# Kernel optimization log

Measured on AMD Instinct MI355X. Metric: run time of the kernel, lower is better.

## Reference

```python
import jax, jax.numpy as jnp
import numpy as np

M_FEATS = 1536      # number of proposals (docstring: [M, K])
K_DIM = 128         # feature dim per docstring example
NUM_CLASSES = 16    # label vocabulary; torch.unique loop becomes a fixed class sweep


def setup_inputs() -> dict:
    key = jax.random.key(0)
    k1, k2 = jax.random.split(key)
    features = jax.random.normal(k1, (M_FEATS, K_DIM), dtype=jnp.float32)
    labels = jax.random.randint(k2, (M_FEATS,), 0, NUM_CLASSES, dtype=jnp.int32)
    # ious all ones -> keep = (ious >= 0.5) is all-True, so the boolean filter is identity
    ious = jnp.ones((M_FEATS,), dtype=jnp.float32)
    return {"features": features, "labels": labels, "ious": ious}


def reference(features, labels, ious):
    # reweight_func='none' -> coef = ones_like(ious); keep mask is all-True by construction
    coef = jnp.ones_like(ious)
    # similarity [M, M]; coef broadcasts over columns, matching `similarity * coef` in torch
    sim = jnp.matmul(features, features.T) * coef[None, :]
    m = sim.shape[0]
    eye = jnp.eye(m, dtype=sim.dtype)
    # ground set term: logdet(similarity + 0.5 I)  (mask_ground is all ones)
    ground = jnp.linalg.slogdet(sim + 0.5 * eye)[1]

    # Per-label logdet of the submatrix S_c + 0.5 I_{n_c}. Instead of extracting a
    # variable-size submatrix (not jit-able), embed it in a full [M, M] matrix that is
    # block-diagonal: class block = S_c + 0.5 I, off-class diagonal = 1. Its logdet
    # equals logdet(S_c + 0.5 I). Absent classes give identity -> logdet 0, matching
    # torch.unique skipping them.
    onehot = (labels[:, None] == jnp.arange(NUM_CLASSES, dtype=labels.dtype)[None, :])
    onehot = onehot.astype(sim.dtype)  # [M, C]

    def class_logdet(mask):  # mask: [M] 0/1 indicator for one class
        A = sim * (mask[:, None] * mask[None, :]) + jnp.diag(0.5 * mask + (1.0 - mask))
        return jnp.linalg.slogdet(A)[1]

    per_class = jax.vmap(class_logdet)(onehot.T)  # [C]
    loss = jnp.sum(per_class) - ground
    return loss  # scalar; .mean() of a scalar is itself
```

## Files before the change

kernel.cpp:

```cpp
#include <hip/hip_runtime.h>
#include <math.h>


#define M_FEATS 1536
#define K_DIM 128
#define NUM_CLASSES 16
#define SLICE 96
#define GRAM_ELEMS (K_DIM * K_DIM)
#define PIDX(i) ((i) + ((i) >> 4))
#define SENT 0x13579BDF

__device__ __forceinline__ float chol128(
    float A[8][8], const int t, const int rg, const int cg,
    const int i0, const int j0,
    float4* panLo, float4* panHi, float4* wshLo, float4* wshHi)
{
    float logsum = 0.0f;

    if (rg == 0) {
#pragma unroll
        for (int q = 0; q < 8; ++q) {
            panLo[PIDX(j0 + q)] = make_float4(A[0][q], A[1][q], A[2][q], A[3][q]);
            panHi[PIDX(j0 + q)] = make_float4(A[4][q], A[5][q], A[6][q], A[7][q]);
        }
    }

#pragma unroll 1
    for (int s = 0; s < 16; ++s) {
        const int k = 8 * s;
        __syncthreads();

        if (t < K_DIM) {
            float4 dL[8], dH[8];
#pragma unroll
            for (int c = 0; c < 8; ++c) {
                dL[c] = panLo[PIDX(k + c)];
                dH[c] = panHi[PIDX(k + c)];
            }
            float4 aL = panLo[PIDX(t)], aH = panHi[PIDX(t)];

            float D[8][8];
#pragma unroll
            for (int c = 0; c < 8; ++c) {
                D[0][c] = dL[c].x; D[1][c] = dL[c].y;
                D[2][c] = dL[c].z; D[3][c] = dL[c].w;
                D[4][c] = dH[c].x; D[5][c] = dH[c].y;
                D[6][c] = dH[c].z; D[7][c] = dH[c].w;
            }

            float L[8][8], ic[8];
            float prod = 1.0f;
#pragma unroll
            for (int c = 0; c < 8; ++c) {
                float v = D[c][c];
#pragma unroll
                for (int m = 0; m < c; ++m) v = fmaf(-L[c][m], L[c][m], v);
                prod *= v;
                ic[c] = rsqrtf(v);
#pragma unroll
                for (int r = c + 1; r < 8; ++r) {
                    float x = D[r][c];
#pragma unroll
                    for (int m = 0; m < c; ++m) x = fmaf(-L[r][m], L[c][m], x);
                    L[r][c] = x * ic[c];
                }
            }
            if (t == 0) logsum += logf(prod);

            float a[8] = {aL.x, aL.y, aL.z, aL.w, aH.x, aH.y, aH.z, aH.w};
            float w[8];
#pragma unroll
            for (int c = 0; c < 8; ++c) {
                float x = a[c];
#pragma unroll
                for (int m = 0; m < c; ++m) x = fmaf(-L[c][m], w[m], x);
                w[c] = x * ic[c];
            }
            wshLo[PIDX(t)] = make_float4(w[0], w[1], w[2], w[3]);
            wshHi[PIDX(t)] = make_float4(w[4], w[5], w[6], w[7]);
        }
        __syncthreads();

        if (rg > s && cg > s) {
            float4 wrL[8], wrH[8];
#pragma unroll
            for (int r = 0; r < 8; ++r) {
                wrL[r] = wshLo[PIDX(i0 + r)];
                wrH[r] = wshHi[PIDX(i0 + r)];
            }
#pragma unroll
            for (int q = 0; q < 8; ++q) {
                float4 wjL = wshLo[PIDX(j0 + q)];
                float4 wjH = wshHi[PIDX(j0 + q)];
#pragma unroll
                for (int r = 0; r < 8; ++r) {
                    float x = A[r][q];
                    x = fmaf(-wrL[r].x, wjL.x, x);
                    x = fmaf(-wrL[r].y, wjL.y, x);
                    x = fmaf(-wrL[r].z, wjL.z, x);
                    x = fmaf(-wrL[r].w, wjL.w, x);
                    x = fmaf(-wrH[r].x, wjH.x, x);
                    x = fmaf(-wrH[r].y, wjH.y, x);
                    x = fmaf(-wrH[r].z, wjH.z, x);
                    x = fmaf(-wrH[r].w, wjH.w, x);
                    A[r][q] = x;
                }
            }
        }
        if (rg == s + 1) {
#pragma unroll
            for (int q = 0; q < 8; ++q) {
                panLo[PIDX(j0 + q)] = make_float4(A[0][q], A[1][q], A[2][q], A[3][q]);
                panHi[PIDX(j0 + q)] = make_float4(A[4][q], A[5][q], A[6][q], A[7][q]);
            }
        }
    }
    return logsum;
}

__global__ __launch_bounds__(256, 1) void fused_kernel(
    const float* __restrict__ f, const int* __restrict__ labels,
    float* __restrict__ partials, float* __restrict__ groundG,
    int* __restrict__ flag1, int* __restrict__ flag2,
    float* __restrict__ ldet, int* __restrict__ flag3,
    float* __restrict__ out)
{
    __shared__ int cnt;
    __shared__ int list[M_FEATS];
    __shared__ float4 panLo[136], panHi[136], wshLo[136], wshHi[136];

    const int b = blockIdx.x;
    const int t = threadIdx.x;
    const int rg = t >> 4;
    const int cg = t & 15;
    const int i0 = rg << 3;
    const int j0 = cg << 3;

    float A[8][8];

    if (b < NUM_CLASSES) {
#pragma unroll
        for (int r = 0; r < 8; ++r)
#pragma unroll
            for (int q = 0; q < 8; ++q) A[r][q] = 0.0f;

        const float* base = f + (size_t)(SLICE * b) * K_DIM;
        float4 A0[3], A1[3], B0[3], B1[3];
#pragma unroll
        for (int u = 0; u < 3; ++u) {
            const float* rp = base + (size_t)u * K_DIM;
            A0[u] = *(const float4*)(rp + i0);
            A1[u] = *(const float4*)(rp + i0 + 4);
            B0[u] = *(const float4*)(rp + j0);
            B1[u] = *(const float4*)(rp + j0 + 4);
        }
        for (int jb = 0; jb < SLICE; jb += 3) {
#pragma unroll
            for (int u = 0; u < 3; ++u) {
                float fa[8] = {A0[u].x, A0[u].y, A0[u].z, A0[u].w,
                               A1[u].x, A1[u].y, A1[u].z, A1[u].w};
                float fb[8] = {B0[u].x, B0[u].y, B0[u].z, B0[u].w,
                               B1[u].x, B1[u].y, B1[u].z, B1[u].w};
#pragma unroll
                for (int r = 0; r < 8; ++r)
#pragma unroll
                    for (int q = 0; q < 8; ++q)
                        A[r][q] = fmaf(fa[r], fb[q], A[r][q]);
                int p = jb + u + 3;
                const float* rp = base + (size_t)(p < SLICE ? p : SLICE - 1) * K_DIM;
                A0[u] = *(const float4*)(rp + i0);
                A1[u] = *(const float4*)(rp + i0 + 4);
                B0[u] = *(const float4*)(rp + j0);
                B1[u] = *(const float4*)(rp + j0 + 4);
            }
        }

        float* g = partials + (size_t)b * GRAM_ELEMS;
#pragma unroll
        for (int r = 0; r < 8; ++r) {
            *(float4*)(g + (i0 + r) * K_DIM + j0) =
                make_float4(A[r][0], A[r][1], A[r][2], A[r][3]);
            *(float4*)(g + (i0 + r) * K_DIM + j0 + 4) =
                make_float4(A[r][4], A[r][5], A[r][6], A[r][7]);
        }
        __syncthreads();
        if (t == 0)
            __hip_atomic_store(&flag1[b], SENT, __ATOMIC_RELEASE,
                               __HIP_MEMORY_SCOPE_AGENT);

        if (t < NUM_CLASSES)
            while (__hip_atomic_load(&flag1[t], __ATOMIC_ACQUIRE,
                                     __HIP_MEMORY_SCOPE_AGENT) != SENT)
                __builtin_amdgcn_s_sleep(2);
        __syncthreads();

        {
            const int row = 8 * b + (t >> 5);
            const int col = (t & 31) << 2;
            float4 s = make_float4(0.f, 0.f, 0.f, 0.f);
#pragma unroll
            for (int c = 0; c < NUM_CLASSES; ++c) {
                float4 v = *(const float4*)(partials + (size_t)c * GRAM_ELEMS
                                            + row * K_DIM + col);
                s.x += v.x; s.y += v.y; s.z += v.z; s.w += v.w;
            }
            *(float4*)(groundG + row * K_DIM + col) = s;
        }
        __syncthreads();
        if (t == 0)
            __hip_atomic_store(&flag2[b], SENT, __ATOMIC_RELEASE,
                               __HIP_MEMORY_SCOPE_AGENT);
        return;
    }

    if (b < 2 * NUM_CLASSES) {
        const int cls = b - NUM_CLASSES;
        if (t == 0) cnt = 0;
        __syncthreads();
        for (int i = t; i < M_FEATS; i += 256)
            if (labels[i] == cls) list[atomicAdd(&cnt, 1)] = i;
        __syncthreads();
        const int n = cnt;

#pragma unroll
        for (int r = 0; r < 8; ++r)
#pragma unroll
            for (int q = 0; q < 8; ++q) A[r][q] = 0.0f;

        if (n > 0) {
            float4 A0[3], A1[3], B0[3], B1[3];
            int lidx[3];
#pragma unroll
            for (int u = 0; u < 3; ++u) {
                const float* rp = f + (size_t)list[u < n ? u : n - 1] * K_DIM;
                A0[u] = *(const float4*)(rp + i0);
                A1[u] = *(const float4*)(rp + i0 + 4);
                B0[u] = *(const float4*)(rp + j0);
                B1[u] = *(const float4*)(rp + j0 + 4);
                const int p = u + 3;
                lidx[u] = list[p < n ? p : n - 1];
            }
            for (int jb = 0; jb < n; jb += 3) {
#pragma unroll
                for (int u = 0; u < 3; ++u) {
                    if (jb + u < n) {
                        float fa[8] = {A0[u].x, A0[u].y, A0[u].z, A0[u].w,
                                       A1[u].x, A1[u].y, A1[u].z, A1[u].w};
                        float fb[8] = {B0[u].x, B0[u].y, B0[u].z, B0[u].w,
                                       B1[u].x, B1[u].y, B1[u].z, B1[u].w};
#pragma unroll
                        for (int r = 0; r < 8; ++r)
#pragma unroll
                            for (int q = 0; q < 8; ++q)
                                A[r][q] = fmaf(fa[r], fb[q], A[r][q]);
                    }
                    const float* rp = f + (size_t)lidx[u] * K_DIM;
                    A0[u] = *(const float4*)(rp + i0);
                    A1[u] = *(const float4*)(rp + i0 + 4);
                    B0[u] = *(const float4*)(rp + j0);
                    B1[u] = *(const float4*)(rp + j0 + 4);
                    const int p = jb + u + 6;
                    lidx[u] = list[p < n ? p : n - 1];
                }
            }
        }

#pragma unroll
        for (int r = 0; r < 8; ++r)
#pragma unroll
            for (int q = 0; q < 8; ++q)
                if ((i0 + r) == (j0 + q)) A[r][q] += 0.5f;

        float ls = chol128(A, t, rg, cg, i0, j0, panLo, panHi, wshLo, wshHi);

        if (t == 0) {
            ldet[cls] = ls;
            __hip_atomic_store(&flag3[cls], SENT, __ATOMIC_RELEASE,
                               __HIP_MEMORY_SCOPE_AGENT);
        }
        return;
    }

    if (t < NUM_CLASSES)
        while (__hip_atomic_load(&flag2[t], __ATOMIC_ACQUIRE,
                                 __HIP_MEMORY_SCOPE_AGENT) != SENT)
            __builtin_amdgcn_s_sleep(2);
    __syncthreads();

#pragma unroll
    for (int r = 0; r < 8; ++r) {
        float4 v0 = *(const float4*)(groundG + (i0 + r) * K_DIM + j0);
        float4 v1 = *(const float4*)(groundG + (i0 + r) * K_DIM + j0 + 4);
        A[r][0] = v0.x; A[r][1] = v0.y; A[r][2] = v0.z; A[r][3] = v0.w;
        A[r][4] = v1.x; A[r][5] = v1.y; A[r][6] = v1.z; A[r][7] = v1.w;
    }
#pragma unroll
    for (int r = 0; r < 8; ++r)
#pragma unroll
        for (int q = 0; q < 8; ++q)
            if ((i0 + r) == (j0 + q)) A[r][q] += 0.5f;

    float ls = chol128(A, t, rg, cg, i0, j0, panLo, panHi, wshLo, wshHi);

    if (t == 0) {
        float total = 1920.0f * 0.6931471805599453f - ls;
        for (int c = 0; c < NUM_CLASSES; ++c) {
            while (__hip_atomic_load(&flag3[c], __ATOMIC_ACQUIRE,
                                     __HIP_MEMORY_SCOPE_AGENT) != SENT)
                __builtin_amdgcn_s_sleep(2);
            total += ldet[c];
        }
        out[0] = total;
    }
}

extern "C" void kernel_launch(void* const* d_in, const int* in_sizes, int n_in,
                              void* d_out, int out_size, void* d_ws, size_t ws_size,
                              hipStream_t stream)
{
    const float* features = (const float*)d_in[0];
    const int* labels = (const int*)d_in[1];

    float* partials = (float*)d_ws;
    float* groundG  = partials + (size_t)NUM_CLASSES * GRAM_ELEMS;
    int* flag1      = (int*)(groundG + GRAM_ELEMS);
    int* flag2      = flag1 + NUM_CLASSES;
    float* ldetp    = (float*)(flag2 + NUM_CLASSES);
    int* flag3      = (int*)(ldetp + NUM_CLASSES);

    fused_kernel<<<2 * NUM_CLASSES + 1, 256, 0, stream>>>(
        features, labels, partials, groundG, flag1, flag2, ldetp, flag3,
        (float*)d_out);
}
```

Baseline: 108.0 us.

## Double threads per block to 512 with 4x8 per-thread tiles in Gram and Cholesky

Each block now runs 512 threads, and each thread holds a 4x8 register tile instead of 8x8. This halves per-thread work in the Gram accumulation and in the Cholesky trailing updates, and the panel write logic is split across pairs of row groups. The final block now polls the per-class flags in parallel instead of serially from one thread. The cost is more synchronization participants per barrier, and the panel-factor stage still uses only 128 threads.

```diff
diff --git a/kernel.cpp b/kernel.cpp
--- a/kernel.cpp
+++ b/kernel.cpp
@@ -11,7 +11,7 @@
 #define SENT 0x13579BDF
 
 __device__ __forceinline__ float chol128(
-    float A[8][8], const int t, const int rg, const int cg,
+    float A[4][8], const int t, const int rg, const int cg,
     const int i0, const int j0,
     float4* panLo, float4* panHi, float4* wshLo, float4* wshHi)
 {
@@ -19,10 +19,12 @@
 
     if (rg == 0) {
 #pragma unroll
-        for (int q = 0; q < 8; ++q) {
+        for (int q = 0; q < 8; ++q)
             panLo[PIDX(j0 + q)] = make_float4(A[0][q], A[1][q], A[2][q], A[3][q]);
-            panHi[PIDX(j0 + q)] = make_float4(A[4][q], A[5][q], A[6][q], A[7][q]);
-        }
+    } else if (rg == 1) {
+#pragma unroll
+        for (int q = 0; q < 8; ++q)
+            panHi[PIDX(j0 + q)] = make_float4(A[0][q], A[1][q], A[2][q], A[3][q]);
     }
 
 #pragma unroll 1
@@ -81,10 +83,10 @@
         }
         __syncthreads();
 
-        if (rg > s && cg > s) {
-            float4 wrL[8], wrH[8];
-#pragma unroll
-            for (int r = 0; r < 8; ++r) {
+        if (rg >= 2 * s + 2 && cg >= s + 1) {
+            float4 wrL[4], wrH[4];
+#pragma unroll
+            for (int r = 0; r < 4; ++r) {
                 wrL[r] = wshLo[PIDX(i0 + r)];
                 wrH[r] = wshHi[PIDX(i0 + r)];
             }
@@ -93,7 +95,7 @@
                 float4 wjL = wshLo[PIDX(j0 + q)];
                 float4 wjH = wshHi[PIDX(j0 + q)];
 #pragma unroll
-                for (int r = 0; r < 8; ++r) {
+                for (int r = 0; r < 4; ++r) {
                     float x = A[r][q];
                     x = fmaf(-wrL[r].x, wjL.x, x);
                     x = fmaf(-wrL[r].y, wjL.y, x);
@@ -107,18 +109,20 @@
                 }
             }
         }
-        if (rg == s + 1) {
-#pragma unroll
-            for (int q = 0; q < 8; ++q) {
+        if (rg == 2 * s + 2) {
+#pragma unroll
+            for (int q = 0; q < 8; ++q)
                 panLo[PIDX(j0 + q)] = make_float4(A[0][q], A[1][q], A[2][q], A[3][q]);
-                panHi[PIDX(j0 + q)] = make_float4(A[4][q], A[5][q], A[6][q], A[7][q]);
-            }
+        } else if (rg == 2 * s + 3) {
+#pragma unroll
+            for (int q = 0; q < 8; ++q)
+                panHi[PIDX(j0 + q)] = make_float4(A[0][q], A[1][q], A[2][q], A[3][q]);
         }
     }
     return logsum;
 }
 
-__global__ __launch_bounds__(256, 1) void fused_kernel(
+__global__ __launch_bounds__(512, 1) void fused_kernel(
     const float* __restrict__ f, const int* __restrict__ labels,
     float* __restrict__ partials, float* __restrict__ groundG,
     int* __restrict__ flag1, int* __restrict__ flag2,
@@ -133,43 +137,40 @@
     const int t = threadIdx.x;
     const int rg = t >> 4;
     const int cg = t & 15;
-    const int i0 = rg << 3;
+    const int i0 = rg << 2;
     const int j0 = cg << 3;
 
-    float A[8][8];
+    float A[4][8];
 
     if (b < NUM_CLASSES) {
 #pragma unroll
-        for (int r = 0; r < 8; ++r)
+        for (int r = 0; r < 4; ++r)
 #pragma unroll
             for (int q = 0; q < 8; ++q) A[r][q] = 0.0f;
 
         const float* base = f + (size_t)(SLICE * b) * K_DIM;
-        float4 A0[3], A1[3], B0[3], B1[3];
+        float4 Ar[3], B0[3], B1[3];
 #pragma unroll
         for (int u = 0; u < 3; ++u) {
             const float* rp = base + (size_t)u * K_DIM;
-            A0[u] = *(const float4*)(rp + i0);
-            A1[u] = *(const float4*)(rp + i0 + 4);
+            Ar[u] = *(const float4*)(rp + i0);
             B0[u] = *(const float4*)(rp + j0);
             B1[u] = *(const float4*)(rp + j0 + 4);
         }
         for (int jb = 0; jb < SLICE; jb += 3) {
 #pragma unroll
             for (int u = 0; u < 3; ++u) {
-                float fa[8] = {A0[u].x, A0[u].y, A0[u].z, A0[u].w,
-                               A1[u].x, A1[u].y, A1[u].z, A1[u].w};
+                float fa[4] = {Ar[u].x, Ar[u].y, Ar[u].z, Ar[u].w};
                 float fb[8] = {B0[u].x, B0[u].y, B0[u].z, B0[u].w,
                                B1[u].x, B1[u].y, B1[u].z, B1[u].w};
 #pragma unroll
-                for (int r = 0; r < 8; ++r)
+                for (int r = 0; r < 4; ++r)
 #pragma unroll
                     for (int q = 0; q < 8; ++q)
                         A[r][q] = fmaf(fa[r], fb[q], A[r][q]);
                 int p = jb + u + 3;
                 const float* rp = base + (size_t)(p < SLICE ? p : SLICE - 1) * K_DIM;
-                A0[u] = *(const float4*)(rp + i0);
-                A1[u] = *(const float4*)(rp + i0 + 4);
+                Ar[u] = *(const float4*)(rp + i0);
                 B0[u] = *(const float4*)(rp + j0);
                 B1[u] = *(const float4*)(rp + j0 + 4);
             }
@@ -177,7 +178,7 @@
 
         float* g = partials + (size_t)b * GRAM_ELEMS;
 #pragma unroll
-        for (int r = 0; r < 8; ++r) {
+        for (int r = 0; r < 4; ++r) {
             *(float4*)(g + (i0 + r) * K_DIM + j0) =
                 make_float4(A[r][0], A[r][1], A[r][2], A[r][3]);
             *(float4*)(g + (i0 + r) * K_DIM + j0 + 4) =
@@ -194,7 +195,7 @@
                 __builtin_amdgcn_s_sleep(2);
         __syncthreads();
 
-        {
+        if (t < 256) {
             const int row = 8 * b + (t >> 5);
             const int col = (t & 31) << 2;
             float4 s = make_float4(0.f, 0.f, 0.f, 0.f);
@@ -217,24 +218,23 @@
         const int cls = b - NUM_CLASSES;
         if (t == 0) cnt = 0;
         __syncthreads();
-        for (int i = t; i < M_FEATS; i += 256)
+        for (int i = t; i < M_FEATS; i += 512)
             if (labels[i] == cls) list[atomicAdd(&cnt, 1)] = i;
         __syncthreads();
         const int n = cnt;
 
 #pragma unroll
-        for (int r = 0; r < 8; ++r)
+        for (int r = 0; r < 4; ++r)
 #pragma unroll
             for (int q = 0; q < 8; ++q) A[r][q] = 0.0f;
 
         if (n > 0) {
-            float4 A0[3], A1[3], B0[3], B1[3];
+            float4 Ar[3], B0[3], B1[3];
             int lidx[3];
 #pragma unroll
             for (int u = 0; u < 3; ++u) {
                 const float* rp = f + (size_t)list[u < n ? u : n - 1] * K_DIM;
-                A0[u] = *(const float4*)(rp + i0);
-                A1[u] = *(const float4*)(rp + i0 + 4);
+                Ar[u] = *(const float4*)(rp + i0);
                 B0[u] = *(const float4*)(rp + j0);
                 B1[u] = *(const float4*)(rp + j0 + 4);
                 const int p = u + 3;
@@ -244,19 +244,17 @@
 #pragma unroll
                 for (int u = 0; u < 3; ++u) {
                     if (jb + u < n) {
-                        float fa[8] = {A0[u].x, A0[u].y, A0[u].z, A0[u].w,
-                                       A1[u].x, A1[u].y, A1[u].z, A1[u].w};
+                        float fa[4] = {Ar[u].x, Ar[u].y, Ar[u].z, Ar[u].w};
                         float fb[8] = {B0[u].x, B0[u].y, B0[u].z, B0[u].w,
                                        B1[u].x, B1[u].y, B1[u].z, B1[u].w};
 #pragma unroll
-                        for (int r = 0; r < 8; ++r)
+                        for (int r = 0; r < 4; ++r)
 #pragma unroll
                             for (int q = 0; q < 8; ++q)
                                 A[r][q] = fmaf(fa[r], fb[q], A[r][q]);
                     }
                     const float* rp = f + (size_t)lidx[u] * K_DIM;
-                    A0[u] = *(const float4*)(rp + i0);
-                    A1[u] = *(const float4*)(rp + i0 + 4);
+                    Ar[u] = *(const float4*)(rp + i0);
                     B0[u] = *(const float4*)(rp + j0);
                     B1[u] = *(const float4*)(rp + j0 + 4);
                     const int p = jb + u + 6;
@@ -266,7 +264,7 @@
         }
 
 #pragma unroll
-        for (int r = 0; r < 8; ++r)
+        for (int r = 0; r < 4; ++r)
 #pragma unroll
             for (int q = 0; q < 8; ++q)
                 if ((i0 + r) == (j0 + q)) A[r][q] += 0.5f;
@@ -288,28 +286,30 @@
     __syncthreads();
 
 #pragma unroll
-    for (int r = 0; r < 8; ++r) {
+    for (int r = 0; r < 4; ++r) {
         float4 v0 = *(const float4*)(groundG + (i0 + r) * K_DIM + j0);
         float4 v1 = *(const float4*)(groundG + (i0 + r) * K_DIM + j0 + 4);
         A[r][0] = v0.x; A[r][1] = v0.y; A[r][2] = v0.z; A[r][3] = v0.w;
         A[r][4] = v1.x; A[r][5] = v1.y; A[r][6] = v1.z; A[r][7] = v1.w;
     }
 #pragma unroll
-    for (int r = 0; r < 8; ++r)
+    for (int r = 0; r < 4; ++r)
 #pragma unroll
         for (int q = 0; q < 8; ++q)
             if ((i0 + r) == (j0 + q)) A[r][q] += 0.5f;
 
     float ls = chol128(A, t, rg, cg, i0, j0, panLo, panHi, wshLo, wshHi);
 
+    if (t < NUM_CLASSES)
+        while (__hip_atomic_load(&flag3[t], __ATOMIC_ACQUIRE,
+                                 __HIP_MEMORY_SCOPE_AGENT) != SENT)
+            __builtin_amdgcn_s_sleep(2);
+    __syncthreads();
+
     if (t == 0) {
         float total = 1920.0f * 0.6931471805599453f - ls;
-        for (int c = 0; c < NUM_CLASSES; ++c) {
-            while (__hip_atomic_load(&flag3[c], __ATOMIC_ACQUIRE,
-                                     __HIP_MEMORY_SCOPE_AGENT) != SENT)
-                __builtin_amdgcn_s_sleep(2);
-            total += ldet[c];
-        }
+#pragma unroll
+        for (int c = 0; c < NUM_CLASSES; ++c) total += ldet[c];
         out[0] = total;
     }
 }
@@ -328,7 +328,7 @@
     float* ldetp    = (float*)(flag2 + NUM_CLASSES);
     int* flag3      = (int*)(ldetp + NUM_CLASSES);
 
-    fused_kernel<<<2 * NUM_CLASSES + 1, 256, 0, stream>>>(
+    fused_kernel<<<2 * NUM_CLASSES + 1, 512, 0, stream>>>(
         features, labels, partials, groundG, flag1, flag2, ldetp, flag3,
         (float*)d_out);
 }
```

Result: faster. 104.2 us (-3.5%).
